# Performance work log

Measured on AMD Instinct MI355X. Metric: run time of the kernel, lower is better.

The kernel has to match this reference:

```python
import jax, jax.numpy as jnp
import numpy as np

NUM_CLASSES = 80
STRIDE = 8
IMG_SIZE = 640
BOX_W, OBJ_W, CLS_W = 7.5, 1.0, 0.5
ANCHORS = jnp.array([[10.0, 13.0], [16.0, 30.0], [33.0, 23.0]], dtype=jnp.float32)
EPS_IOU = 1e-9
EPS_CIOU = 1e-7


def setup_inputs() -> dict:
    key = jax.random.key(0)
    k1, k2, k3 = jax.random.split(key, 3)
    B, na, H, W, D = 16, 3, 80, 80, 5 + NUM_CLASSES
    N = 48  # objects per image
    p_raw = jax.random.normal(k1, (B, na, H, W, D), dtype=jnp.float32)
    labels_xywh = jax.random.uniform(k2, (B, N, 4), dtype=jnp.float32)  # normalized (xc,yc,w,h)
    labels_cls = jax.random.randint(k3, (B, N), 0, NUM_CLASSES, dtype=jnp.int32)
    return {"p_raw": p_raw, "labels_xywh": labels_xywh, "labels_cls": labels_cls}


def _assign_targets(labels_cls, labels_xywh, B, na, H, W):
    lab = labels_xywh * IMG_SIZE  # [B,N,4] in pixels
    gx, gy, gw, gh = lab[..., 0], lab[..., 1], lab[..., 2], lab[..., 3]
    gi_idx = jnp.clip(gx / STRIDE, 0, W - 0.001).astype(jnp.int32)  # [B,N]
    gj_idx = jnp.clip(gy / STRIDE, 0, H - 0.001).astype(jnp.int32)
    a_wh = ANCHORS / STRIDE  # [na,2] anchors in grid units
    gtw, gth = gw / STRIDE, gh / STRIDE
    inter = jnp.minimum(gtw[..., None], a_wh[:, 0]) * jnp.minimum(gth[..., None], a_wh[:, 1])
    union = gtw[..., None] * gth[..., None] + a_wh[:, 0] * a_wh[:, 1] - inter + EPS_IOU
    best_a = jnp.argmax(inter / union, axis=-1).astype(jnp.int32)  # [B,N]

    # 3x3 neighborhood offsets (di over x, dj over y), matching torch loop order
    offs = jnp.array([(di, dj) for di in (-1, 0, 1) for dj in (-1, 0, 1)], dtype=jnp.int32)  # [9,2]
    bidx = jnp.arange(B, dtype=jnp.int32)

    tobj = jnp.zeros((B, na, H, W), dtype=jnp.float32)
    tcls = jnp.zeros((B, na, H, W, NUM_CLASSES), dtype=jnp.float32)
    tbox = jnp.zeros((B, na, H, W, 4), dtype=jnp.float32)

    def step(carry, x):
        tobj, tcls, tbox = carry
        a, gi, gj, c, box = x  # a,gi,gj,c: [B]; box: [B,4]
        ii = jnp.clip(gi[:, None] + offs[None, :, 0], 0, W - 1)  # [B,9]
        jj = jnp.clip(gj[:, None] + offs[None, :, 1], 0, H - 1)  # [B,9]
        b9 = jnp.broadcast_to(bidx[:, None], (B, 9))
        a9 = jnp.broadcast_to(a[:, None], (B, 9))
        c9 = jnp.broadcast_to(c[:, None], (B, 9))
        tobj = tobj.at[b9, a9, jj, ii].set(1.0)
        tcls = tcls.at[b9, a9, jj, ii, c9].set(1.0)
        tbox = tbox.at[b9, a9, jj, ii].set(jnp.broadcast_to(box[:, None, :], (B, 9, 4)))
        return (tobj, tcls, tbox), None

    xs = (best_a.T, gi_idx.T, gj_idx.T, labels_cls.T, jnp.swapaxes(lab, 0, 1))
    (tobj, tcls, tbox), _ = jax.lax.scan(step, (tobj, tcls, tbox), xs)
    return tobj, tcls, tbox


def _ciou(pred, tgt):
    # pred, tgt: [..., 4] (xc, yc, w, h) in pixels
    px, py, pw, ph = pred[..., 0], pred[..., 1], pred[..., 2], pred[..., 3]
    gx, gy, gw, gh = tgt[..., 0], tgt[..., 1], tgt[..., 2], tgt[..., 3]
    px1, py1, px2, py2 = px - pw / 2, py - ph / 2, px + pw / 2, py + ph / 2
    gx1, gy1, gx2, gy2 = gx - gw / 2, gy - gh / 2, gx + gw / 2, gy + gh / 2
    iw = jnp.clip(jnp.minimum(px2, gx2) - jnp.maximum(px1, gx1), 0)
    ih = jnp.clip(jnp.minimum(py2, gy2) - jnp.maximum(py1, gy1), 0)
    inter = iw * ih
    area_p = jnp.clip(px2 - px1, 0) * jnp.clip(py2 - py1, 0)
    area_g = jnp.clip(gx2 - gx1, 0) * jnp.clip(gy2 - gy1, 0)
    union = area_p + area_g - inter + EPS_CIOU
    iou = inter / union
    cw = jnp.clip(jnp.maximum(px2, gx2) - jnp.minimum(px1, gx1), 0)
    ch = jnp.clip(jnp.maximum(py2, gy2) - jnp.minimum(py1, gy1), 0)
    c2 = cw * cw + ch * ch + EPS_CIOU
    rho2 = (px - gx) ** 2 + (py - gy) ** 2
    v = (4.0 / (np.pi ** 2)) * (jnp.arctan(gw / (gh + EPS_CIOU)) - jnp.arctan(pw / (ph + EPS_CIOU))) ** 2
    alpha = jax.lax.stop_gradient(v / (1 - iou + v + EPS_CIOU))
    return 1 - (iou - rho2 / c2 - alpha * v)


def _bce_logits(x, t):
    # stable binary cross-entropy with logits: softplus(x) - t*x
    return jax.nn.softplus(x) - t * x


def reference(p_raw, labels_xywh, labels_cls):
    B, na, H, W, D = p_raw.shape
    ag = ANCHORS / STRIDE  # anchors in grid units
    px = jax.nn.sigmoid(p_raw[..., 0])
    py = jax.nn.sigmoid(p_raw[..., 1])
    pw = jnp.exp(p_raw[..., 2]) * ag[:, 0][None, :, None, None]
    ph = jnp.exp(p_raw[..., 3]) * ag[:, 1][None, :, None, None]
    logits_obj = p_raw[..., 4]
    logits_cls = p_raw[..., 5:]

    gyv, gxv = jnp.meshgrid(jnp.arange(H, dtype=jnp.float32), jnp.arange(W, dtype=jnp.float32), indexing='ij')
    gx = (gxv[None, None] + px) * STRIDE
    gy = (gyv[None, None] + py) * STRIDE
    pxywh = jnp.stack([gx, gy, pw * STRIDE, ph * STRIDE], -1)  # [B,na,H,W,4]

    tobj, tcls, tbox = _assign_targets(labels_cls, labels_xywh, B, na, H, W)
    pos = tobj > 0.5
    n_pos = jnp.maximum(jnp.sum(pos), 1).astype(jnp.float32)

    ciou = _ciou(pxywh, tbox)  # [B,na,H,W]
    l_box = jnp.sum(jnp.where(pos, ciou, 0.0)) / n_pos
    l_obj = jnp.mean(_bce_logits(logits_obj, tobj))
    bce_cls = _bce_logits(logits_cls, tcls)  # [B,na,H,W,nc]
    l_cls = jnp.sum(jnp.where(pos[..., None], bce_cls, 0.0)) / (n_pos * NUM_CLASSES)

    total = BOX_W * l_box + OBJ_W * l_obj + CLS_W * l_cls
    return total
```

## Files before the change

kernel.cpp:

```cpp
#include <hip/hip_runtime.h>

#define NC    80
#define B_    16
#define NA    3
#define HW    80
#define D_    85
#define NLAB  48
#define NCELL  (B_*NA*HW*HW)
#define OBJBLK (NCELL/256)
#define POSBLK (B_*108)
#define NBLK_T (OBJBLK+POSBLK)

__device__ __forceinline__ float softplusf(float x) {
    return fmaxf(x, 0.f) + log1pf(expf(-fabsf(x)));
}
__device__ __forceinline__ int clampi(int v, int lo, int hi) {
    return min(max(v, lo), hi);
}

__global__ __launch_bounds__(256) void k_main(const float* __restrict__ p,
                                              const float* __restrict__ lx,
                                              const int*   __restrict__ lc,
                                              float* __restrict__ opart,
                                              float* __restrict__ ppart) {
    int t = threadIdx.x, bid = blockIdx.x;
    int lane = t & 63, wid = t >> 6;
    __shared__ float r4[4][4];

    if (bid < OBJBLK) {
        int idx = bid * 256 + t;
        float s = softplusf(p[(size_t)idx * D_ + 4]);
        #pragma unroll
        for (int o = 32; o; o >>= 1) s += __shfl_xor(s, o);
        if (lane == 0) r4[wid][0] = s;
        __syncthreads();
        if (t == 0) opart[bid] = r4[0][0] + r4[1][0] + r4[2][0] + r4[3][0];
        return;
    }

    int pb = bid - OBJBLK;
    int b  = pb / 108;

    __shared__ float Lgx[NLAB], Lgy[NLAB], Lgw[NLAB], Lgh[NLAB];
    __shared__ int   Lgi[NLAB], Lgj[NLAB], La[NLAB], Lc[NLAB];

    if (t < NLAB) {
        float4 L = ((const float4*)lx)[b * NLAB + t];
        float gx = L.x * 640.f, gy = L.y * 640.f;
        float gw = L.z * 640.f, gh = L.w * 640.f;
        Lgx[t] = gx; Lgy[t] = gy; Lgw[t] = gw; Lgh[t] = gh;
        Lgi[t] = (int)fminf(fmaxf(gx * 0.125f, 0.f), 79.999f);
        Lgj[t] = (int)fminf(fmaxf(gy * 0.125f, 0.f), 79.999f);
        float gtw = gw * 0.125f, gth = gh * 0.125f;
        const float aw[3] = {1.25f, 2.0f, 4.125f};
        const float ah[3] = {1.625f, 3.75f, 2.875f};
        int a = 0; float best = -1.f;
        #pragma unroll
        for (int k = 0; k < 3; k++) {
            float inter = fminf(gtw, aw[k]) * fminf(gth, ah[k]);
            float uni   = gtw * gth + aw[k] * ah[k] - inter + 1e-9f;
            float r = inter / uni;
            if (r > best) { best = r; a = k; }
        }
        La[t] = a;
        Lc[t] = lc[b * NLAB + t];
    }
    __syncthreads();

    int cand = (pb % 108) * 4 + wid;
    int n = cand / 9, off = cand % 9;
    int gi = Lgi[n], gj = Lgj[n], a = La[n];
    int ii = clampi(gi + off / 3 - 1, 0, 79);
    int jj = clampi(gj + off % 3 - 1, 0, 79);

    bool viol = false;
    if (lane < 9) {
        if (lane < off) {
            int i2 = clampi(gi + lane / 3 - 1, 0, 79);
            int j2 = clampi(gj + lane % 3 - 1, 0, 79);
            viol = (i2 == ii) && (j2 == jj);
        }
    } else {
        int n2 = n + 1 + (lane - 9);
        if (n2 < NLAB && La[n2] == a) {
            int g2 = Lgi[n2], h2 = Lgj[n2];
            viol = ii >= max(g2 - 1, 0) && ii <= min(g2 + 1, 79) &&
                   jj >= max(h2 - 1, 0) && jj <= min(h2 + 1, 79);
        }
    }
    bool own = (__ballot(viol) == 0ull);

    float box = 0.f, cls = 0.f, xc = 0.f, npf = 0.f;
    if (own) {
        int cell = ((b * NA + a) * HW + jj) * HW + ii;
        const float* pc = p + (size_t)cell * D_;
        int c = Lc[n];

        float x = pc[5 + lane];
        float cs = softplusf(x) - ((lane == c) ? x : 0.f);
        if (lane < 16) {
            float x2 = pc[69 + lane];
            cs += softplusf(x2) - ((lane + 64 == c) ? x2 : 0.f);
        }
        #pragma unroll
        for (int o = 32; o; o >>= 1) cs += __shfl_xor(cs, o);

        if (lane == 0) {
            npf = 1.f;
            cls = cs;
            xc  = pc[4];

            float awv = (a == 0) ? 10.f : ((a == 1) ? 16.f : 33.f);
            float ahv = (a == 0) ? 13.f : ((a == 1) ? 30.f : 23.f);
            float p0 = pc[0], p1 = pc[1], p2 = pc[2], p3 = pc[3];
            float sx = 1.f / (1.f + expf(-p0));
            float sy = 1.f / (1.f + expf(-p1));
            float px = ((float)ii + sx) * 8.f;
            float py = ((float)jj + sy) * 8.f;
            float pw = expf(p2) * awv;
            float ph = expf(p3) * ahv;

            float gx = Lgx[n], gy = Lgy[n], gw = Lgw[n], gh = Lgh[n];

            float px1 = px - pw * 0.5f, px2 = px + pw * 0.5f;
            float py1 = py - ph * 0.5f, py2 = py + ph * 0.5f;
            float gx1 = gx - gw * 0.5f, gx2 = gx + gw * 0.5f;
            float gy1 = gy - gh * 0.5f, gy2 = gy + gh * 0.5f;

            float iw = fmaxf(fminf(px2, gx2) - fmaxf(px1, gx1), 0.f);
            float ih = fmaxf(fminf(py2, gy2) - fmaxf(py1, gy1), 0.f);
            float inter = iw * ih;
            float ap = fmaxf(px2 - px1, 0.f) * fmaxf(py2 - py1, 0.f);
            float ag = fmaxf(gx2 - gx1, 0.f) * fmaxf(gy2 - gy1, 0.f);
            float uni = ap + ag - inter + 1e-7f;
            float iou = inter / uni;

            float cw = fmaxf(fmaxf(px2, gx2) - fminf(px1, gx1), 0.f);
            float ch = fmaxf(fmaxf(py2, gy2) - fminf(py1, gy1), 0.f);
            float c2 = cw * cw + ch * ch + 1e-7f;
            float rho2 = (px - gx) * (px - gx) + (py - gy) * (py - gy);

            float dv = atanf(gw / (gh + 1e-7f)) - atanf(pw / (ph + 1e-7f));
            float v = 0.40528473456935108577f * dv * dv;
            float alpha = v / (1.f - iou + v + 1e-7f);
            box = 1.f - (iou - rho2 / c2 - alpha * v);
        }
    }

    if (lane == 0) { r4[wid][0] = box; r4[wid][1] = cls; r4[wid][2] = xc; r4[wid][3] = npf; }
    __syncthreads();
    if (t == 0) {
        float4 o;
        o.x = r4[0][0] + r4[1][0] + r4[2][0] + r4[3][0];
        o.y = r4[0][1] + r4[1][1] + r4[2][1] + r4[3][1];
        o.z = r4[0][2] + r4[1][2] + r4[2][2] + r4[3][2];
        o.w = r4[0][3] + r4[1][3] + r4[2][3] + r4[3][3];
        ((float4*)ppart)[pb] = o;
    }
}

__global__ __launch_bounds__(256) void k_fin(const float* __restrict__ opart,
                                             const float* __restrict__ ppart,
                                             float* __restrict__ out) {
    int t = threadIdx.x, lane = t & 63, wid = t >> 6;
    float o = 0.f, box = 0.f, cls = 0.f, xc = 0.f, np = 0.f;
    #pragma unroll
    for (int k = 0; k < 5; k++) {
        int i = t + k * 256;
        if (i < OBJBLK) o += opart[i];
    }
    #pragma unroll
    for (int k = 0; k < 7; k++) {
        int i = t + k * 256;
        if (i < POSBLK) {
            float4 v = ((const float4*)ppart)[i];
            box += v.x; cls += v.y; xc += v.z; np += v.w;
        }
    }
    #pragma unroll
    for (int s = 32; s; s >>= 1) {
        o   += __shfl_xor(o,   s);
        box += __shfl_xor(box, s);
        cls += __shfl_xor(cls, s);
        xc  += __shfl_xor(xc,  s);
        np  += __shfl_xor(np,  s);
    }
    __shared__ float r[4][5];
    if (lane == 0) { r[wid][0]=o; r[wid][1]=box; r[wid][2]=cls; r[wid][3]=xc; r[wid][4]=np; }
    __syncthreads();
    if (t == 0) {
        float O  = r[0][0] + r[1][0] + r[2][0] + r[3][0];
        float Bx = r[0][1] + r[1][1] + r[2][1] + r[3][1];
        float Cl = r[0][2] + r[1][2] + r[2][2] + r[3][2];
        float Xc = r[0][3] + r[1][3] + r[2][3] + r[3][3];
        float Np = r[0][4] + r[1][4] + r[2][4] + r[3][4];
        float npos = fmaxf(Np, 1.f);
        out[0] = 7.5f * Bx / npos
               + (O - Xc) / (float)NCELL
               + 0.5f * Cl / (npos * (float)NC);
    }
}

extern "C" void kernel_launch(void* const* d_in, const int* in_sizes, int n_in,
                              void* d_out, int out_size, void* d_ws, size_t ws_size,
                              hipStream_t stream) {
    const float* p  = (const float*)d_in[0];
    const float* lx = (const float*)d_in[1];
    const int*   lc = (const int*)d_in[2];
    float*       out = (float*)d_out;

    float* opart = (float*)d_ws;
    float* ppart = (float*)((char*)d_ws + 8192);

    k_main<<<NBLK_T, 256, 0, stream>>>(p, lx, lc, opart, ppart);
    k_fin<<<1, 256, 0, stream>>>(opart, ppart, out);
}
```

Before: 23.13 us.

## Stream whole prediction tensor with coalesced float4 loads for objectness softplus sum

Replaces the per-cell strided read of the objectness logit with a grid-stride loop that reads the entire prediction tensor as float4 and picks out the objectness lanes via a modulo-85 position test. The intent is to turn scattered single-float loads into fully coalesced streaming loads. It reads every byte of the tensor instead of one float per cell, and accumulates in double precision with double partials in the finalize kernel.

After: 44.54 us. +92.6%, slower.

```diff
diff --git a/kernel.cpp b/kernel.cpp
--- a/kernel.cpp
+++ b/kernel.cpp
@@ -7,9 +7,12 @@
 #define D_    85
 #define NLAB  48
 #define NCELL  (B_*NA*HW*HW)
-#define OBJBLK (NCELL/256)
+#define N4     6528000
+#define STRBLK 832
+#define STRTHR (STRBLK*256)
+#define NFULL  30
 #define POSBLK (B_*108)
-#define NBLK_T (OBJBLK+POSBLK)
+#define NBLK_T (STRBLK+POSBLK)
 
 __device__ __forceinline__ float softplusf(float x) {
     return fmaxf(x, 0.f) + log1pf(expf(-fabsf(x)));
@@ -21,24 +24,51 @@
 __global__ __launch_bounds__(256) void k_main(const float* __restrict__ p,
                                               const float* __restrict__ lx,
                                               const int*   __restrict__ lc,
-                                              float* __restrict__ opart,
-                                              float* __restrict__ ppart) {
+                                              double* __restrict__ opart,
+                                              float*  __restrict__ ppart) {
     int t = threadIdx.x, bid = blockIdx.x;
     int lane = t & 63, wid = t >> 6;
-    __shared__ float r4[4][4];
-
-    if (bid < OBJBLK) {
-        int idx = bid * 256 + t;
-        float s = softplusf(p[(size_t)idx * D_ + 4]);
+    __shared__ float  r4[4][4];
+    __shared__ double wd[4];
+
+    if (bid < STRBLK) {
+        const float4* __restrict__ p4 = (const float4*)p;
+        int tid = bid * 256 + t;
+        double s = 0.0;
+        #pragma unroll 5
+        for (int k = 0; k < NFULL; k++) {
+            int i = tid + k * STRTHR;
+            float4 v = p4[i];
+            unsigned r = (4u * (unsigned)i + 81u) % 85u;
+            float val = (r == 0u)  ? v.x :
+                        (r == 84u) ? v.y :
+                        (r == 83u) ? v.z :
+                        (r == 82u) ? v.w : 0.f;
+            bool m = (r == 0u) || (r >= 82u);
+            s += m ? (double)softplusf(val) : 0.0;
+        }
+        {
+            int i = tid + NFULL * STRTHR;
+            if (i < N4) {
+                float4 v = p4[i];
+                unsigned r = (4u * (unsigned)i + 81u) % 85u;
+                float val = (r == 0u)  ? v.x :
+                            (r == 84u) ? v.y :
+                            (r == 83u) ? v.z :
+                            (r == 82u) ? v.w : 0.f;
+                bool m = (r == 0u) || (r >= 82u);
+                s += m ? (double)softplusf(val) : 0.0;
+            }
+        }
         #pragma unroll
         for (int o = 32; o; o >>= 1) s += __shfl_xor(s, o);
-        if (lane == 0) r4[wid][0] = s;
+        if (lane == 0) wd[wid] = s;
         __syncthreads();
-        if (t == 0) opart[bid] = r4[0][0] + r4[1][0] + r4[2][0] + r4[3][0];
+        if (t == 0) opart[bid] = wd[0] + wd[1] + wd[2] + wd[3];
         return;
     }
 
-    int pb = bid - OBJBLK;
+    int pb = bid - STRBLK;
     int b  = pb / 108;
 
     __shared__ float Lgx[NLAB], Lgy[NLAB], Lgw[NLAB], Lgh[NLAB];
@@ -159,16 +189,17 @@
     }
 }
 
-__global__ __launch_bounds__(256) void k_fin(const float* __restrict__ opart,
-                                             const float* __restrict__ ppart,
+__global__ __launch_bounds__(256) void k_fin(const double* __restrict__ opart,
+                                             const float*  __restrict__ ppart,
                                              float* __restrict__ out) {
     int t = threadIdx.x, lane = t & 63, wid = t >> 6;
-    float o = 0.f, box = 0.f, cls = 0.f, xc = 0.f, np = 0.f;
+    double o = 0.0;
     #pragma unroll
-    for (int k = 0; k < 5; k++) {
+    for (int k = 0; k < 4; k++) {
         int i = t + k * 256;
-        if (i < OBJBLK) o += opart[i];
-    }
+        if (i < STRBLK) o += opart[i];
+    }
+    float box = 0.f, cls = 0.f, xc = 0.f, np = 0.f;
     #pragma unroll
     for (int k = 0; k < 7; k++) {
         int i = t + k * 256;
@@ -185,19 +216,22 @@
         xc  += __shfl_xor(xc,  s);
         np  += __shfl_xor(np,  s);
     }
-    __shared__ float r[4][5];
-    if (lane == 0) { r[wid][0]=o; r[wid][1]=box; r[wid][2]=cls; r[wid][3]=xc; r[wid][4]=np; }
+    __shared__ double so[4];
+    __shared__ float  r[4][4];
+    if (lane == 0) {
+        so[wid] = o;
+        r[wid][0]=box; r[wid][1]=cls; r[wid][2]=xc; r[wid][3]=np;
+    }
     __syncthreads();
     if (t == 0) {
-        float O  = r[0][0] + r[1][0] + r[2][0] + r[3][0];
-        float Bx = r[0][1] + r[1][1] + r[2][1] + r[3][1];
-        float Cl = r[0][2] + r[1][2] + r[2][2] + r[3][2];
-        float Xc = r[0][3] + r[1][3] + r[2][3] + r[3][3];
-        float Np = r[0][4] + r[1][4] + r[2][4] + r[3][4];
+        double O = so[0] + so[1] + so[2] + so[3];
+        float Bx = r[0][0] + r[1][0] + r[2][0] + r[3][0];
+        float Cl = r[0][1] + r[1][1] + r[2][1] + r[3][1];
+        float Xc = r[0][2] + r[1][2] + r[2][2] + r[3][2];
+        float Np = r[0][3] + r[1][3] + r[2][3] + r[3][3];
         float npos = fmaxf(Np, 1.f);
-        out[0] = 7.5f * Bx / npos
-               + (O - Xc) / (float)NCELL
-               + 0.5f * Cl / (npos * (float)NC);
+        float lobj = (float)((O - (double)Xc) / (double)NCELL);
+        out[0] = 7.5f * Bx / npos + lobj + 0.5f * Cl / (npos * (float)NC);
     }
 }
 
@@ -209,8 +243,8 @@
     const int*   lc = (const int*)d_in[2];
     float*       out = (float*)d_out;
 
-    float* opart = (float*)d_ws;
-    float* ppart = (float*)((char*)d_ws + 8192);
+    double* opart = (double*)d_ws;
+    float*  ppart = (float*)((char*)d_ws + 8192);
 
     k_main<<<NBLK_T, 256, 0, stream>>>(p, lx, lc, opart, ppart);
     k_fin<<<1, 256, 0, stream>>>(opart, ppart, out);
```
